# Optimization experiments

Measured on AMD Instinct MI355X. Metric: run time of the kernel, lower is better.

The kernel has to match this reference:

```python
import jax, jax.numpy as jnp
import numpy as np
from jax import lax

ENC_DIM, DEC_DIM, ATT_DIM, CONV_CH, KSIZE, ATT_ODIM = 1024, 1024, 512, 32, 50, 1024
SCALING = 2.0


def setup_inputs() -> dict:
    key = jax.random.key(0)
    ks = jax.random.split(key, 12)
    B, T = 32, 2000
    enc_pad = jax.random.normal(ks[0], (B, T, ENC_DIM), dtype=jnp.float32)
    enc_len = jax.random.randint(ks[1], (B,), 1000, T + 1, dtype=jnp.int32)
    dec_h = jax.random.normal(ks[2], (B, 1, DEC_DIM), dtype=jnp.float32)
    att_prev = jax.random.uniform(ks[3], (B, T), dtype=jnp.float32)
    s = 0.02
    W_enc = jax.random.normal(ks[4], (ENC_DIM, ATT_DIM), dtype=jnp.float32) * s
    b_enc = jnp.zeros((ATT_DIM,), jnp.float32)
    W_dec = jax.random.normal(ks[5], (DEC_DIM, ATT_DIM), dtype=jnp.float32) * s
    b_dec = jnp.zeros((ATT_DIM,), jnp.float32)
    W_att = jax.random.normal(ks[6], (CONV_CH, ATT_DIM), dtype=jnp.float32) * s
    b_att = jnp.zeros((ATT_DIM,), jnp.float32)
    # Conv2d(1, C, kernel=(1, 2K+1)) acting on (B,1,1,T) == 1D conv kernel (C,1,2K+1)
    conv_w = jax.random.normal(ks[7], (CONV_CH, 1, 2 * KSIZE + 1), dtype=jnp.float32) * s
    gvec = jax.random.normal(ks[8], (ATT_DIM, 1), dtype=jnp.float32) * s
    W_o = jax.random.normal(ks[9], (ENC_DIM, ATT_ODIM), dtype=jnp.float32) * s
    b_o = jnp.zeros((ATT_ODIM,), jnp.float32)
    return {"enc_pad": enc_pad, "enc_len": enc_len, "dec_h": dec_h, "att_prev": att_prev,
            "W_enc": W_enc, "b_enc": b_enc, "W_dec": W_dec, "b_dec": b_dec,
            "W_att": W_att, "b_att": b_att, "conv_w": conv_w, "gvec": gvec,
            "W_o": W_o, "b_o": b_o}


def reference(enc_pad, enc_len, dec_h, att_prev, W_enc, b_enc, W_dec, b_dec,
              W_att, b_att, conv_w, gvec, W_o, b_o):
    B, T, _ = enc_pad.shape
    enc_h = enc_pad @ W_enc + b_enc                           # [B,T,A]
    # location conv: (B,1,T) * (C,1,K) -> (B,C,T), SAME padding
    att_conv = lax.conv_general_dilated(
        att_prev[:, None, :], conv_w, window_strides=(1,),
        padding=[(KSIZE, KSIZE)], dimension_numbers=("NCH", "OIH", "NCH"))
    att_conv = jnp.transpose(att_conv, (0, 2, 1)) @ W_att + b_att  # [B,T,A]
    dec_term = (dec_h.reshape(B, DEC_DIM) @ W_dec + b_dec)[:, None, :]  # [B,1,A]
    att_state = jnp.tanh(enc_h + dec_term + att_conv)         # [B,T,A]
    e = (att_state @ gvec)[:, :, 0]                           # [B,T]
    mask = jnp.arange(T)[None, :] >= enc_len[:, None]         # True = padded
    e = jnp.where(mask, jnp.float32(-1e15), e)
    attn = jax.nn.softmax(SCALING * e, axis=1)                # [B,T]
    c = jnp.einsum("bt,btd->bd", attn, enc_pad)               # [B,enc_dim]
    c = c @ W_o + b_o                                         # [B,att_odim]
    return c, attn
```

## Files before the change

### kernel.cpp

```cpp
#include <hip/hip_runtime.h>
#include <stdint.h>
#include <stddef.h>

#define T_LEN   2000
#define BATCH   32
#define ROWS    64000
#define KDIM    1024
#define ADIM    512
#define CCH     32
#define KW      101

typedef _Float16 half8_t  __attribute__((ext_vector_type(8)));
typedef float    float4_t __attribute__((ext_vector_type(4)));

__device__ __forceinline__ half8_t pack8(float4_t a, float4_t b) {
    half8_t r;
    r[0] = (_Float16)a.x; r[1] = (_Float16)a.y;
    r[2] = (_Float16)a.z; r[3] = (_Float16)a.w;
    r[4] = (_Float16)b.x; r[5] = (_Float16)b.y;
    r[6] = (_Float16)b.z; r[7] = (_Float16)b.w;
    return r;
}

__device__ __forceinline__ float tanh_fast(float x) {
    float ax = __builtin_fabsf(x);
    ax = fminf(ax, 15.f);
    float e = __expf(2.f * ax);
    float t = 1.f - 2.f / (e + 1.f);
    return (x < 0.f) ? -t : t;
}

#define OFF_WENCT 0
#define OFF_WATTT 1048576
#define OFF_CONVA 1081344
#define OFF_DTERM 5177344
#define OFF_EPART 5242880
#define OFF_CPART 6266880

__global__ __launch_bounds__(256) void k_prep_w(const float* __restrict__ We,
                                                const float* __restrict__ Wa,
                                                _Float16* __restrict__ Wet,
                                                _Float16* __restrict__ Wat) {
    int id = blockIdx.x * 256 + threadIdx.x;
    if (id < ADIM * KDIM) {
        int n = id >> 10, k = id & 1023;
        Wet[id] = (_Float16)We[k * ADIM + n];
    } else {
        int id2 = id - ADIM * KDIM;
        if (id2 < ADIM * CCH) {
            int n = id2 >> 5, c = id2 & 31;
            Wat[id2] = (_Float16)Wa[c * ADIM + n];
        }
    }
}

__global__ __launch_bounds__(512) void k_dterm(const float* __restrict__ dec_h,
                                               const float* __restrict__ W_dec,
                                               const float* __restrict__ be,
                                               const float* __restrict__ bd,
                                               const float* __restrict__ ba,
                                               float* __restrict__ dterm) {
    __shared__ float dh[KDIM];
    int b = blockIdx.x;
    for (int k = threadIdx.x; k < KDIM; k += 512) dh[k] = dec_h[b * KDIM + k];
    __syncthreads();
    int a = threadIdx.x;
    float s = be[a] + bd[a] + ba[a];
    for (int k = 0; k < KDIM; ++k) s += dh[k] * W_dec[k * ADIM + a];
    dterm[b * ADIM + a] = s;
}

__global__ __launch_bounds__(256) void k_conv(const float* __restrict__ att_prev,
                                              const float* __restrict__ conv_w,
                                              _Float16* __restrict__ convA) {
    __shared__ float ap[128 + 100];
    __shared__ float w[CCH * KW];
    int b = blockIdx.y, tt = blockIdx.x;
    int t0 = tt * 128;
    for (int i = threadIdx.x; i < 228; i += 256) {
        int t = t0 - 50 + i;
        ap[i] = (t >= 0 && t < T_LEN) ? att_prev[b * T_LEN + t] : 0.f;
    }
    for (int i = threadIdx.x; i < CCH * KW; i += 256) w[i] = conv_w[i];
    __syncthreads();
    for (int idx = threadIdx.x; idx < 128 * CCH; idx += 256) {
        int tl = idx >> 5, c = idx & 31;
        int t = t0 + tl;
        if (t < T_LEN) {
            float s = 0.f;
            for (int j = 0; j < KW; ++j) s += ap[tl + j] * w[c * KW + j];
            convA[(size_t)(b * T_LEN + t) * CCH + c] = (_Float16)s;
        }
    }
}

__global__ __launch_bounds__(256) void k_gemm_e(const float* __restrict__ enc,
                                                const _Float16* __restrict__ Wet,
                                                const _Float16* __restrict__ convA,
                                                const _Float16* __restrict__ Wat,
                                                const float* __restrict__ dterm,
                                                const float* __restrict__ gvec,
                                                float* __restrict__ epart) {
    __shared__ __attribute__((aligned(16))) _Float16 Ah[128 * 32];
    __shared__ __attribute__((aligned(16))) _Float16 Bh[128 * 32];

    const int tid  = threadIdx.x;
    const int nc   = blockIdx.x;
    const int m0   = blockIdx.y * 128;
    const int wave = tid >> 6, lane = tid & 63;
    const int quad = lane >> 4, c16 = lane & 15;
    const int wm = (wave >> 1) * 64, wn = (wave & 1) * 64;

    float4_t acc[4][4];
#pragma unroll
    for (int i = 0; i < 4; ++i)
#pragma unroll
        for (int j = 0; j < 4; ++j) acc[i][j] = (float4_t){0.f, 0.f, 0.f, 0.f};

    const int srow = tid >> 1, shalf = tid & 1;
    const float*    aSrc = enc + (size_t)(m0 + srow) * KDIM + shalf * 16;
    const _Float16* bSrc = Wet + (size_t)(nc * 128 + srow) * KDIM + shalf * 16;
    const int ldsOff = srow * 32 + shalf * 16;

    for (int kk = 0; kk < 32; ++kk) {
        const int k0 = kk * 32;
        __syncthreads();
        {
            const float4_t* s = (const float4_t*)(aSrc + k0);
            float4_t v0 = s[0], v1 = s[1], v2 = s[2], v3 = s[3];
            *(half8_t*)&Ah[ldsOff]     = pack8(v0, v1);
            *(half8_t*)&Ah[ldsOff + 8] = pack8(v2, v3);
            const half8_t* bs = (const half8_t*)(bSrc + k0);
            *(half8_t*)&Bh[ldsOff]     = bs[0];
            *(half8_t*)&Bh[ldsOff + 8] = bs[1];
        }
        __syncthreads();
        half8_t af[4], bf[4];
#pragma unroll
        for (int i = 0; i < 4; ++i)
            af[i] = *(const half8_t*)&Ah[(wm + i * 16 + c16) * 32 + quad * 8];
#pragma unroll
        for (int j = 0; j < 4; ++j)
            bf[j] = *(const half8_t*)&Bh[(wn + j * 16 + c16) * 32 + quad * 8];
#pragma unroll
        for (int i = 0; i < 4; ++i)
#pragma unroll
            for (int j = 0; j < 4; ++j)
                acc[i][j] = __builtin_amdgcn_mfma_f32_16x16x32_f16(af[i], bf[j], acc[i][j], 0, 0, 0);
    }

    __syncthreads();
    {
        const half8_t* as = (const half8_t*)(convA + (size_t)(m0 + srow) * CCH + shalf * 16);
        *(half8_t*)&Ah[ldsOff]     = as[0];
        *(half8_t*)&Ah[ldsOff + 8] = as[1];
        const half8_t* bs = (const half8_t*)(Wat + (size_t)(nc * 128 + srow) * CCH + shalf * 16);
        *(half8_t*)&Bh[ldsOff]     = bs[0];
        *(half8_t*)&Bh[ldsOff + 8] = bs[1];
    }
    __syncthreads();
    {
        half8_t af[4], bf[4];
#pragma unroll
        for (int i = 0; i < 4; ++i)
            af[i] = *(const half8_t*)&Ah[(wm + i * 16 + c16) * 32 + quad * 8];
#pragma unroll
        for (int j = 0; j < 4; ++j)
            bf[j] = *(const half8_t*)&Bh[(wn + j * 16 + c16) * 32 + quad * 8];
#pragma unroll
        for (int i = 0; i < 4; ++i)
#pragma unroll
            for (int j = 0; j < 4; ++j)
                acc[i][j] = __builtin_amdgcn_mfma_f32_16x16x32_f16(af[i], bf[j], acc[i][j], 0, 0, 0);
    }

    __syncthreads();
    float* e_lds = (float*)Ah;
#pragma unroll
    for (int i = 0; i < 4; ++i) {
        const int rl0 = wm + i * 16 + quad * 4;
#pragma unroll
        for (int r = 0; r < 4; ++r) {
            const int grow = m0 + rl0 + r;
            const int b = grow / T_LEN;
            float s = 0.f;
#pragma unroll
            for (int j = 0; j < 4; ++j) {
                const int col = nc * 128 + wn + j * 16 + c16;
                const float v = acc[i][j][r] + dterm[b * ADIM + col];
                s += tanh_fast(v) * gvec[col];
            }
#pragma unroll
            for (int off = 1; off < 16; off <<= 1) s += __shfl_xor(s, off);
            if (c16 == 0) e_lds[(wave & 1) * 128 + rl0 + r] = s;
        }
    }
    __syncthreads();
    if (tid < 128) epart[nc * ROWS + m0 + tid] = e_lds[tid] + e_lds[128 + tid];
}

__global__ __launch_bounds__(512) void k_softmax(const float* __restrict__ epart,
                                                 const int* __restrict__ enc_len,
                                                 float* __restrict__ attn) {
    __shared__ float ex[T_LEN];
    __shared__ float red[8];
    const int b = blockIdx.x, tid = threadIdx.x;
    const int len = enc_len[b];
    float lmax = -3.4e38f;
    for (int t = tid; t < T_LEN; t += 512) {
        float e = epart[b * T_LEN + t] + epart[ROWS + b * T_LEN + t]
                + epart[2 * ROWS + b * T_LEN + t] + epart[3 * ROWS + b * T_LEN + t];
        float lg = (t < len) ? 2.f * e : -2e15f;
        ex[t] = lg;
        lmax = fmaxf(lmax, lg);
    }
    for (int off = 1; off < 64; off <<= 1) lmax = fmaxf(lmax, __shfl_xor(lmax, off));
    if ((tid & 63) == 0) red[tid >> 6] = lmax;
    __syncthreads();
    const float m = fmaxf(fmaxf(fmaxf(red[0], red[1]), fmaxf(red[2], red[3])),
                          fmaxf(fmaxf(red[4], red[5]), fmaxf(red[6], red[7])));
    float lsum = 0.f;
    for (int t = tid; t < T_LEN; t += 512) {
        float p = __expf(ex[t] - m);
        ex[t] = p;
        lsum += p;
    }
    for (int off = 1; off < 64; off <<= 1) lsum += __shfl_xor(lsum, off);
    __syncthreads();
    if ((tid & 63) == 0) red[tid >> 6] = lsum;
    __syncthreads();
    const float inv = 1.f / (red[0] + red[1] + red[2] + red[3] + red[4] + red[5] + red[6] + red[7]);
    for (int t = tid; t < T_LEN; t += 512) attn[b * T_LEN + t] = ex[t] * inv;
}

__global__ __launch_bounds__(256) void k_cpart(const float* __restrict__ attn,
                                               const float* __restrict__ enc,
                                               float* __restrict__ cpart) {
    const int b = blockIdx.y, tc = blockIdx.x, tid = threadIdx.x;
    const int t0 = tc * 125;
    float4_t s = (float4_t){0.f, 0.f, 0.f, 0.f};
    const float4_t* ep = (const float4_t*)(enc + (size_t)b * T_LEN * KDIM) + tid;
    const float* ap = attn + b * T_LEN + t0;
#pragma unroll 5
    for (int tt = 0; tt < 125; ++tt) {
        const float w = ap[tt];
        float4_t v = ep[(size_t)(t0 + tt) * 256];
        s += v * w;
    }
    *(float4_t*)&cpart[(size_t)(tc * BATCH + b) * KDIM + tid * 4] = s;
}

__global__ __launch_bounds__(512) void k_out(const float* __restrict__ cpart,
                                             const float* __restrict__ W_o,
                                             const float* __restrict__ b_o,
                                             float* __restrict__ out_c) {
    __shared__ float cm[KDIM];
    const int b = blockIdx.x, tid = threadIdx.x;
    for (int d = tid; d < KDIM; d += 512) {
        float s = 0.f;
#pragma unroll
        for (int p = 0; p < 16; ++p) s += cpart[(size_t)(p * BATCH + b) * KDIM + d];
        cm[d] = s;
    }
    __syncthreads();
    for (int o = tid; o < KDIM; o += 512) {
        float s = b_o[o];
        for (int d = 0; d < KDIM; ++d) s += cm[d] * W_o[d * KDIM + o];
        out_c[b * KDIM + o] = s;
    }
}

extern "C" void kernel_launch(void* const* d_in, const int* in_sizes, int n_in,
                              void* d_out, int out_size, void* d_ws, size_t ws_size,
                              hipStream_t stream) {
    const float* enc      = (const float*)d_in[0];
    const int*   enc_len  = (const int*)d_in[1];
    const float* dec_h    = (const float*)d_in[2];
    const float* att_prev = (const float*)d_in[3];
    const float* W_enc    = (const float*)d_in[4];
    const float* b_enc    = (const float*)d_in[5];
    const float* W_dec    = (const float*)d_in[6];
    const float* b_dec    = (const float*)d_in[7];
    const float* W_att    = (const float*)d_in[8];
    const float* b_att    = (const float*)d_in[9];
    const float* conv_w   = (const float*)d_in[10];
    const float* gvec     = (const float*)d_in[11];
    const float* W_o      = (const float*)d_in[12];
    const float* b_o      = (const float*)d_in[13];

    float* out_c    = (float*)d_out;
    float* out_attn = out_c + BATCH * KDIM;

    char* ws = (char*)d_ws;
    _Float16* Wet   = (_Float16*)(ws + OFF_WENCT);
    _Float16* Wat   = (_Float16*)(ws + OFF_WATTT);
    _Float16* convA = (_Float16*)(ws + OFF_CONVA);
    float*    dterm = (float*)(ws + OFF_DTERM);
    float*    epart = (float*)(ws + OFF_EPART);
    float*    cpart = (float*)(ws + OFF_CPART);

    k_prep_w<<<2112, 256, 0, stream>>>(W_enc, W_att, Wet, Wat);
    k_dterm<<<BATCH, 512, 0, stream>>>(dec_h, W_dec, b_enc, b_dec, b_att, dterm);
    k_conv<<<dim3(16, BATCH), 256, 0, stream>>>(att_prev, conv_w, convA);
    k_gemm_e<<<dim3(4, 500), 256, 0, stream>>>(enc, Wet, convA, Wat, dterm, gvec, epart);
    k_softmax<<<BATCH, 512, 0, stream>>>(epart, enc_len, out_attn);
    k_cpart<<<dim3(16, BATCH), 256, 0, stream>>>(out_attn, enc, cpart);
    k_out<<<BATCH, 512, 0, stream>>>(cpart, W_o, b_o, out_c);
}
```

Baseline: 683.5 us.

## Widen GEMM tile to full N, prefetch A, async B loads, parallelize small kernels

The main GEMM now lets each 512-thread block cover all 512 output columns for 128 rows. The fp32 encoder input is therefore read and converted once rather than four times across column blocks, and the cross-block e partial sums are removed. It also register-prefetches the next A tile, loads B directly into LDS with global_load_lds, and pads the A LDS rows to reduce bank conflicts. The weight transpose uses a shared-memory tile, and dterm and the output projection are split across more blocks. The trade-offs are higher register use (acc 4x8, occupancy 1) and only 500 blocks for the GPU's CUs.

After: 628.0 us. 1.09x faster.

```diff
diff --git a/kernel.cpp b/kernel.cpp
--- a/kernel.cpp
+++ b/kernel.cpp
@@ -9,6 +9,7 @@
 #define ADIM    512
 #define CCH     32
 #define KW      101
+#define PADA    40
 
 typedef _Float16 half8_t  __attribute__((ext_vector_type(8)));
 typedef float    float4_t __attribute__((ext_vector_type(4)));
@@ -30,44 +31,63 @@
     return (x < 0.f) ? -t : t;
 }
 
+__device__ __forceinline__ void glds16(const void* g, void* l) {
+    __builtin_amdgcn_global_load_lds((const __attribute__((address_space(1))) uint32_t*)g,
+                                     (__attribute__((address_space(3))) uint32_t*)l,
+                                     16, 0, 0);
+}
+
 #define OFF_WENCT 0
 #define OFF_WATTT 1048576
 #define OFF_CONVA 1081344
 #define OFF_DTERM 5177344
 #define OFF_EPART 5242880
-#define OFF_CPART 6266880
-
-__global__ __launch_bounds__(256) void k_prep_w(const float* __restrict__ We,
-                                                const float* __restrict__ Wa,
-                                                _Float16* __restrict__ Wet,
-                                                _Float16* __restrict__ Wat) {
-    int id = blockIdx.x * 256 + threadIdx.x;
-    if (id < ADIM * KDIM) {
-        int n = id >> 10, k = id & 1023;
-        Wet[id] = (_Float16)We[k * ADIM + n];
-    } else {
-        int id2 = id - ADIM * KDIM;
-        if (id2 < ADIM * CCH) {
-            int n = id2 >> 5, c = id2 & 31;
-            Wat[id2] = (_Float16)Wa[c * ADIM + n];
-        }
-    }
-}
-
-__global__ __launch_bounds__(512) void k_dterm(const float* __restrict__ dec_h,
+#define OFF_CPART 5498880
+
+__global__ __launch_bounds__(256) void k_prep_we(const float* __restrict__ We,
+                                                 _Float16* __restrict__ Wet) {
+    __shared__ float tile[32][33];
+    const int k0 = blockIdx.x * 32, n0 = blockIdx.y * 32;
+    const int tx = threadIdx.x & 31, ty = threadIdx.x >> 5;
+#pragma unroll
+    for (int i = 0; i < 4; ++i)
+        tile[ty + i * 8][tx] = We[(size_t)(k0 + ty + i * 8) * ADIM + n0 + tx];
+    __syncthreads();
+#pragma unroll
+    for (int i = 0; i < 4; ++i)
+        Wet[(size_t)(n0 + ty + i * 8) * KDIM + k0 + tx] = (_Float16)tile[tx][ty + i * 8];
+}
+
+__global__ __launch_bounds__(512) void k_prep_wat(const float* __restrict__ Wa,
+                                                  _Float16* __restrict__ Wat) {
+    const int n = threadIdx.x;
+#pragma unroll
+    for (int c = 0; c < CCH; ++c)
+        Wat[n * CCH + c] = (_Float16)Wa[c * ADIM + n];
+}
+
+__global__ __launch_bounds__(256) void k_dterm(const float* __restrict__ dec_h,
                                                const float* __restrict__ W_dec,
                                                const float* __restrict__ be,
                                                const float* __restrict__ bd,
                                                const float* __restrict__ ba,
                                                float* __restrict__ dterm) {
     __shared__ float dh[KDIM];
-    int b = blockIdx.x;
-    for (int k = threadIdx.x; k < KDIM; k += 512) dh[k] = dec_h[b * KDIM + k];
-    __syncthreads();
-    int a = threadIdx.x;
-    float s = be[a] + bd[a] + ba[a];
-    for (int k = 0; k < KDIM; ++k) s += dh[k] * W_dec[k * ADIM + a];
-    dterm[b * ADIM + a] = s;
+    __shared__ float part[256];
+    const int b = blockIdx.x, a0 = blockIdx.y * 128, tid = threadIdx.x;
+#pragma unroll
+    for (int i = 0; i < 4; ++i) dh[tid + i * 256] = dec_h[b * KDIM + tid + i * 256];
+    __syncthreads();
+    const int a = a0 + (tid & 127), kh = (tid >> 7) * 512;
+    float s = 0.f;
+#pragma unroll 8
+    for (int k = 0; k < 512; ++k) s += dh[kh + k] * W_dec[(size_t)(kh + k) * ADIM + a];
+    part[tid] = s;
+    __syncthreads();
+    if (tid < 128) {
+        const int aa = a0 + tid;
+        dterm[b * ADIM + aa] = part[tid] + part[tid + 128] + be[aa] + bd[aa] + ba[aa];
+    }
 }
 
 __global__ __launch_bounds__(256) void k_conv(const float* __restrict__ att_prev,
@@ -88,89 +108,92 @@
         int t = t0 + tl;
         if (t < T_LEN) {
             float s = 0.f;
+#pragma unroll
             for (int j = 0; j < KW; ++j) s += ap[tl + j] * w[c * KW + j];
             convA[(size_t)(b * T_LEN + t) * CCH + c] = (_Float16)s;
         }
     }
 }
 
-__global__ __launch_bounds__(256) void k_gemm_e(const float* __restrict__ enc,
-                                                const _Float16* __restrict__ Wet,
-                                                const _Float16* __restrict__ convA,
-                                                const _Float16* __restrict__ Wat,
-                                                const float* __restrict__ dterm,
-                                                const float* __restrict__ gvec,
-                                                float* __restrict__ epart) {
-    __shared__ __attribute__((aligned(16))) _Float16 Ah[128 * 32];
-    __shared__ __attribute__((aligned(16))) _Float16 Bh[128 * 32];
+__global__ __launch_bounds__(512, 1) void k_gemm_e(const float* __restrict__ enc,
+                                                   const _Float16* __restrict__ Wet,
+                                                   const _Float16* __restrict__ convA,
+                                                   const _Float16* __restrict__ Wat,
+                                                   const float* __restrict__ dterm,
+                                                   const float* __restrict__ gvec,
+                                                   float* __restrict__ epart) {
+    __shared__ __attribute__((aligned(16))) _Float16 Ah[128 * PADA];
+    __shared__ __attribute__((aligned(16))) _Float16 Bh[512 * 32];
 
     const int tid  = threadIdx.x;
-    const int nc   = blockIdx.x;
-    const int m0   = blockIdx.y * 128;
+    const int m0   = blockIdx.x * 128;
     const int wave = tid >> 6, lane = tid & 63;
     const int quad = lane >> 4, c16 = lane & 15;
-    const int wm = (wave >> 1) * 64, wn = (wave & 1) * 64;
-
-    float4_t acc[4][4];
+    const int wm = (wave >> 2) * 64, wn = (wave & 3) * 128;
+
+    float4_t acc[4][8];
 #pragma unroll
     for (int i = 0; i < 4; ++i)
 #pragma unroll
-        for (int j = 0; j < 4; ++j) acc[i][j] = (float4_t){0.f, 0.f, 0.f, 0.f};
-
-    const int srow = tid >> 1, shalf = tid & 1;
-    const float*    aSrc = enc + (size_t)(m0 + srow) * KDIM + shalf * 16;
-    const _Float16* bSrc = Wet + (size_t)(nc * 128 + srow) * KDIM + shalf * 16;
-    const int ldsOff = srow * 32 + shalf * 16;
+        for (int j = 0; j < 8; ++j) acc[i][j] = (float4_t){0.f, 0.f, 0.f, 0.f};
+
+    const int arow = tid >> 2, aseg = tid & 3;
+    const float* aBase = enc + (size_t)(m0 + arow) * KDIM + aseg * 8;
+    const int bl4 = lane >> 2, bseg = lane & 3;
+
+    float4_t pa0 = ((const float4_t*)aBase)[0];
+    float4_t pa1 = ((const float4_t*)aBase)[1];
 
     for (int kk = 0; kk < 32; ++kk) {
         const int k0 = kk * 32;
         __syncthreads();
-        {
-            const float4_t* s = (const float4_t*)(aSrc + k0);
-            float4_t v0 = s[0], v1 = s[1], v2 = s[2], v3 = s[3];
-            *(half8_t*)&Ah[ldsOff]     = pack8(v0, v1);
-            *(half8_t*)&Ah[ldsOff + 8] = pack8(v2, v3);
-            const half8_t* bs = (const half8_t*)(bSrc + k0);
-            *(half8_t*)&Bh[ldsOff]     = bs[0];
-            *(half8_t*)&Bh[ldsOff + 8] = bs[1];
+        *(half8_t*)&Ah[arow * PADA + aseg * 8] = pack8(pa0, pa1);
+#pragma unroll
+        for (int p = 0; p < 4; ++p) {
+            const int nb = wave * 64 + p * 16 + bl4;
+            glds16(Wet + (size_t)nb * KDIM + k0 + bseg * 8, &Bh[nb * 32 + bseg * 8]);
         }
         __syncthreads();
-        half8_t af[4], bf[4];
+        {
+            const int kn = (kk < 31) ? (k0 + 32) : k0;
+            pa0 = ((const float4_t*)(aBase + kn))[0];
+            pa1 = ((const float4_t*)(aBase + kn))[1];
+        }
+        half8_t af[4], bf[8];
 #pragma unroll
         for (int i = 0; i < 4; ++i)
-            af[i] = *(const half8_t*)&Ah[(wm + i * 16 + c16) * 32 + quad * 8];
-#pragma unroll
-        for (int j = 0; j < 4; ++j)
+            af[i] = *(const half8_t*)&Ah[(wm + i * 16 + c16) * PADA + quad * 8];
+#pragma unroll
+        for (int j = 0; j < 8; ++j)
             bf[j] = *(const half8_t*)&Bh[(wn + j * 16 + c16) * 32 + quad * 8];
 #pragma unroll
         for (int i = 0; i < 4; ++i)
 #pragma unroll
-            for (int j = 0; j < 4; ++j)
+            for (int j = 0; j < 8; ++j)
                 acc[i][j] = __builtin_amdgcn_mfma_f32_16x16x32_f16(af[i], bf[j], acc[i][j], 0, 0, 0);
     }
 
     __syncthreads();
+    *(half8_t*)&Ah[arow * PADA + aseg * 8] =
+        *(const half8_t*)(convA + (size_t)(m0 + arow) * CCH + aseg * 8);
     {
-        const half8_t* as = (const half8_t*)(convA + (size_t)(m0 + srow) * CCH + shalf * 16);
-        *(half8_t*)&Ah[ldsOff]     = as[0];
-        *(half8_t*)&Ah[ldsOff + 8] = as[1];
-        const half8_t* bs = (const half8_t*)(Wat + (size_t)(nc * 128 + srow) * CCH + shalf * 16);
-        *(half8_t*)&Bh[ldsOff]     = bs[0];
-        *(half8_t*)&Bh[ldsOff + 8] = bs[1];
+        const half8_t* bs = (const half8_t*)(Wat + tid * CCH);
+#pragma unroll
+        for (int s4 = 0; s4 < 4; ++s4) *(half8_t*)&Bh[tid * 32 + s4 * 8] = bs[s4];
     }
     __syncthreads();
     {
-        half8_t af[4], bf[4];
+        half8_t af[4], bf[8];
 #pragma unroll
         for (int i = 0; i < 4; ++i)
-            af[i] = *(const half8_t*)&Ah[(wm + i * 16 + c16) * 32 + quad * 8];
-#pragma unroll
-        for (int j = 0; j < 4; ++j)
+            af[i] = *(const half8_t*)&Ah[(wm + i * 16 + c16) * PADA + quad * 8];
+#pragma unroll
+        for (int j = 0; j < 8; ++j)
             bf[j] = *(const half8_t*)&Bh[(wn + j * 16 + c16) * 32 + quad * 8];
 #pragma unroll
         for (int i = 0; i < 4; ++i)
 #pragma unroll
-            for (int j = 0; j < 4; ++j)
+            for (int j = 0; j < 8; ++j)
                 acc[i][j] = __builtin_amdgcn_mfma_f32_16x16x32_f16(af[i], bf[j], acc[i][j], 0, 0, 0);
     }
 
@@ -185,18 +208,21 @@
             const int b = grow / T_LEN;
             float s = 0.f;
 #pragma unroll
-            for (int j = 0; j < 4; ++j) {
-                const int col = nc * 128 + wn + j * 16 + c16;
+            for (int j = 0; j < 8; ++j) {
+                const int col = wn + j * 16 + c16;
                 const float v = acc[i][j][r] + dterm[b * ADIM + col];
                 s += tanh_fast(v) * gvec[col];
             }
 #pragma unroll
             for (int off = 1; off < 16; off <<= 1) s += __shfl_xor(s, off);
-            if (c16 == 0) e_lds[(wave & 1) * 128 + rl0 + r] = s;
+            if (c16 == 0) e_lds[(rl0 + r) * 4 + (wave & 3)] = s;
         }
     }
     __syncthreads();
-    if (tid < 128) epart[nc * ROWS + m0 + tid] = e_lds[tid] + e_lds[128 + tid];
+    if (tid < 128) {
+        float4_t q = ((const float4_t*)e_lds)[tid];
+        epart[m0 + tid] = q.x + q.y + q.z + q.w;
+    }
 }
 
 __global__ __launch_bounds__(512) void k_softmax(const float* __restrict__ epart,
@@ -208,9 +234,7 @@
     const int len = enc_len[b];
     float lmax = -3.4e38f;
     for (int t = tid; t < T_LEN; t += 512) {
-        float e = epart[b * T_LEN + t] + epart[ROWS + b * T_LEN + t]
-                + epart[2 * ROWS + b * T_LEN + t] + epart[3 * ROWS + b * T_LEN + t];
-        float lg = (t < len) ? 2.f * e : -2e15f;
+        float lg = (t < len) ? 2.f * epart[b * T_LEN + t] : -2e15f;
         ex[t] = lg;
         lmax = fmaxf(lmax, lg);
     }
@@ -250,24 +274,24 @@
     *(float4_t*)&cpart[(size_t)(tc * BATCH + b) * KDIM + tid * 4] = s;
 }
 
-__global__ __launch_bounds__(512) void k_out(const float* __restrict__ cpart,
+__global__ __launch_bounds__(256) void k_out(const float* __restrict__ cpart,
                                              const float* __restrict__ W_o,
                                              const float* __restrict__ b_o,
                                              float* __restrict__ out_c) {
     __shared__ float cm[KDIM];
     const int b = blockIdx.x, tid = threadIdx.x;
-    for (int d = tid; d < KDIM; d += 512) {
+    for (int d = tid; d < KDIM; d += 256) {
         float s = 0.f;
 #pragma unroll
         for (int p = 0; p < 16; ++p) s += cpart[(size_t)(p * BATCH + b) * KDIM + d];
         cm[d] = s;
     }
     __syncthreads();
-    for (int o = tid; o < KDIM; o += 512) {
-        float s = b_o[o];
-        for (int d = 0; d < KDIM; ++d) s += cm[d] * W_o[d * KDIM + o];
-        out_c[b * KDIM + o] = s;
-    }
+    const int o = blockIdx.y * 256 + tid;
+    float s = b_o[o];
+#pragma unroll 8
+    for (int d = 0; d < KDIM; ++d) s += cm[d] * W_o[(size_t)d * KDIM + o];
+    out_c[b * KDIM + o] = s;
 }
 
 extern "C" void kernel_launch(void* const* d_in, const int* in_sizes, int n_in,
@@ -299,11 +323,12 @@
     float*    epart = (float*)(ws + OFF_EPART);
     float*    cpart = (float*)(ws + OFF_CPART);
 
-    k_prep_w<<<2112, 256, 0, stream>>>(W_enc, W_att, Wet, Wat);
-    k_dterm<<<BATCH, 512, 0, stream>>>(dec_h, W_dec, b_enc, b_dec, b_att, dterm);
+    k_prep_we<<<dim3(32, 16), 256, 0, stream>>>(W_enc, Wet);
+    k_prep_wat<<<1, 512, 0, stream>>>(W_att, Wat);
+    k_dterm<<<dim3(BATCH, 4), 256, 0, stream>>>(dec_h, W_dec, b_enc, b_dec, b_att, dterm);
     k_conv<<<dim3(16, BATCH), 256, 0, stream>>>(att_prev, conv_w, convA);
-    k_gemm_e<<<dim3(4, 500), 256, 0, stream>>>(enc, Wet, convA, Wat, dterm, gvec, epart);
+    k_gemm_e<<<500, 512, 0, stream>>>(enc, Wet, convA, Wat, dterm, gvec, epart);
     k_softmax<<<BATCH, 512, 0, stream>>>(epart, enc_len, out_attn);
     k_cpart<<<dim3(16, BATCH), 256, 0, stream>>>(out_attn, enc, cpart);
-    k_out<<<BATCH, 512, 0, stream>>>(cpart, W_o, b_o, out_c);
-}
+    k_out<<<dim3(BATCH, 4), 256, 0, stream>>>(cpart, W_o, b_o, out_c);
+}
```
